# Kernel tuning notes

Measured on AMD Instinct MI355X. Metric: run time of the kernel, lower is better.

The kernel has to match this reference:

```python
import jax, jax.numpy as jnp
import numpy as np
import math

HEADS = 8
DIM_HEAD = 64


def setup_inputs() -> dict:
    key = jax.random.key(0)
    k1, k2, k3 = jax.random.split(key, 3)
    b, n, dim = 4, 2048, 512
    inner = HEADS * DIM_HEAD  # 512
    x = jax.random.normal(k1, (b, n, dim), dtype=jnp.float32)
    W_qkv = jax.random.normal(k2, (dim, 4 * inner), dtype=jnp.float32) * (dim ** -0.5)
    W_out = jax.random.normal(k3, (2 * inner, dim), dtype=jnp.float32) * ((2 * inner) ** -0.5)
    b_out = jnp.zeros((dim,), dtype=jnp.float32)
    return {"x": x, "W_qkv": W_qkv, "W_out": W_out, "b_out": b_out}


def reference(x, W_qkv, W_out, b_out):
    b, n, d = x.shape
    h, dh = HEADS, DIM_HEAD
    scale = dh ** -0.5
    qkvt = x @ W_qkv  # [b, n, 4*h*dh]
    q, k, v, t = jnp.split(qkvt, 4, axis=-1)
    # 'b n (h d) -> b h n d'
    def to_heads(z):
        return z.reshape(b, n, h, dh).transpose(0, 2, 1, 3)
    q, k, v, t = map(to_heads, (q, k, v, t))

    # Branch 1: standard softmax attention
    dots = jnp.einsum('bhid,bhjd->bhij', q, k) * scale
    attn1 = jax.nn.softmax(dots, axis=-1)
    out1 = jnp.einsum('bhij,bhjd->bhid', attn1, v)

    # Branch 2: fixed positional-decay attention (shared across b, h; no repeat needed)
    pos = jnp.arange(1, n + 1, dtype=x.dtype)  # linspace(1, n, n)
    tg = jnp.abs(pos[None, :] - pos[:, None])  # |j - i|, [n, n]
    attn2 = jnp.exp(-tg / jnp.asarray(math.e, dtype=x.dtype))
    # NOTE: original divides by sum(-1) WITHOUT keepdim -> broadcasts over columns:
    # attn2[i, j] / sum_k attn2[j, k]
    attn2 = attn2 / attn2.sum(-1)
    out2 = jnp.einsum('ij,bhjd->bhid', attn2, t)

    out = jnp.concatenate([out1, out2], axis=-1)  # [b, h, n, 2*dh]
    out = out.transpose(0, 2, 1, 3).reshape(b, n, 2 * h * dh)  # 'b h n d -> b n (h d)'
    return out @ W_out + b_out
```

## Files before the change

kernel.cpp:

```cpp
#include <hip/hip_runtime.h>
#include <hip/hip_bf16.h>

#define B_ 4
#define N_ 2048
#define D_ 512
#define H_ 8
#define DH_ 64

typedef float float4_ __attribute__((ext_vector_type(4)));
typedef int int2_ __attribute__((ext_vector_type(2)));
typedef int int4_ __attribute__((ext_vector_type(4)));
typedef unsigned short ushort4_ __attribute__((ext_vector_type(4)));
typedef unsigned short ushort8_ __attribute__((ext_vector_type(8)));
typedef __bf16 bf16x8 __attribute__((ext_vector_type(8)));
typedef _Float16 half2_ __attribute__((ext_vector_type(2)));
typedef _Float16 half4_ __attribute__((ext_vector_type(4)));
typedef _Float16 half8_ __attribute__((ext_vector_type(8)));

#if __has_builtin(__builtin_amdgcn_exp2f)
#define EXP2(x) __builtin_amdgcn_exp2f(x)
#else
#define EXP2(x) exp2f(x)
#endif

__device__ __forceinline__ float b2f(unsigned short u) {
  union { unsigned int u; float f; } v; v.u = ((unsigned int)u) << 16; return v.f;
}
__device__ __forceinline__ unsigned short f2b(float f) {
  union { float f; unsigned int u; } v; v.f = f;
  unsigned int r = v.u + 0x7fffu + ((v.u >> 16) & 1u);
  return (unsigned short)(r >> 16);
}
__device__ __forceinline__ half4_ pk4(float a, float b, float c, float d) {
  half2_ lo = __builtin_bit_cast(half2_, __builtin_amdgcn_cvt_pkrtz(a, b));
  half2_ hi = __builtin_bit_cast(half2_, __builtin_amdgcn_cvt_pkrtz(c, d));
  return __builtin_bit_cast(half4_,
      (int2_){__builtin_bit_cast(int, lo), __builtin_bit_cast(int, hi)});
}

#define GLD16(gp, lp)                                                        \
  __builtin_amdgcn_global_load_lds(                                          \
      (const __attribute__((address_space(1))) unsigned int*)(gp),           \
      (__attribute__((address_space(3))) unsigned int*)(lp), 16, 0, 0)

__device__ __forceinline__ bool detect_fp32_local(
    const unsigned short* __restrict__ xhdr, int* cnt_sh) {
  if (threadIdx.x == 0) *cnt_sh = 0;
  __syncthreads();
  unsigned int e = (xhdr[threadIdx.x] >> 7) & 0xFFu;
  if (e >= 134u) atomicAdd(cnt_sh, 1);
  __syncthreads();
  return *cnt_sh > 16;
}

__device__ __forceinline__ void transpose_conv(
    const void* __restrict__ src, unsigned short* __restrict__ dst,
    int R, int C, int bx, int by, bool ofp) {
  __shared__ unsigned short tile[32][33];
  const int c0 = bx * 32, r0 = by * 32;
  const int tx = threadIdx.x & 31, ty = threadIdx.x >> 5;
#pragma unroll
  for (int k = 0; k < 4; ++k) {
    int r = ty + k * 8;
    long idx = (long)(r0 + r) * C + c0 + tx;
    tile[r][tx] = ofp ? f2b(((const float*)src)[idx])
                      : ((const unsigned short*)src)[idx];
  }
  __syncthreads();
#pragma unroll
  for (int k = 0; k < 4; ++k) {
    int c = ty + k * 8;
    dst[(long)(c0 + c) * R + r0 + tx] = tile[tx][c];
  }
}

__global__ __launch_bounds__(256) void prep_all(
    const void* __restrict__ xraw, const void* __restrict__ Wqraw,
    const void* __restrict__ Woraw, unsigned short* __restrict__ xb,
    unsigned short* __restrict__ WqT, unsigned short* __restrict__ WoT,
    unsigned short* __restrict__ Wband) {
  __shared__ int cnt_sh;
  const bool ofp = detect_fp32_local((const unsigned short*)xraw, &cnt_sh);
  const int bid = blockIdx.x;
  if (bid < 4096) {
    int i4 = bid * 256 + threadIdx.x;
    ushort4_ o;
    if (ofp) {
      float4_ v = ((const float4_*)xraw)[i4];
      o[0] = f2b(v[0]); o[1] = f2b(v[1]); o[2] = f2b(v[2]); o[3] = f2b(v[3]);
    } else {
      o = ((const ushort4_*)xraw)[i4];
    }
    *(ushort4_*)(xb + (long)i4 * 4) = o;
  } else if (bid < 5120) {
    const int b2 = bid - 4096;
    transpose_conv(Wqraw, WqT, 512, 2048, b2 % 64, b2 / 64, ofp);
  } else if (bid < 5632) {
    const int b2 = bid - 5120;
    transpose_conv(Woraw, WoT, 1024, 512, b2 % 16, b2 / 16, ofp);
  } else {
    constexpr float INV_E = 0.36787944117144233f;
    constexpr float R1 = 0.69220062755534635f;
    constexpr float INV_1MR = 3.2488706f;
    const int i = bid - 5632;
    const int krel = threadIdx.x;
    const int j = (i >> 6) * 64 - 96 + krel;
    float c = 0.f;
    if (j >= 0 && j < N_) {
      float wgt = __expf(-fabsf((float)(i - j)) * INV_E);
      float rj = __expf(-(float)j * INV_E);
      float rnj = __expf(-(float)(N_ - 1 - j) * INV_E);
      float S = 1.f + R1 * (2.f - rj - rnj) * INV_1MR;
      c = wgt / S;
    }
    _Float16 hv = (_Float16)c;
    Wband[i * 256 + krel] = __builtin_bit_cast(unsigned short, hv);
  }
}

#define MFMA16x32(d, a, b) \
  d = __builtin_amdgcn_mfma_f32_16x16x32_bf16(a, b, d, 0, 0, 0)

__global__ __launch_bounds__(512, 2) void gemm256(
    const unsigned short* __restrict__ A, const unsigned short* __restrict__ Bt,
    unsigned short* __restrict__ C, int M, int N, int K) {
  __shared__ unsigned short As[2][16384];
  __shared__ unsigned short Bs[2][16384];
  const int tid = threadIdx.x;
  const int w = tid >> 6, lane = tid & 63, l16 = lane & 15, quad = lane >> 4;
  const int wm = w >> 2, wn = w & 3;
  const long tm = (long)blockIdx.x * 256, tn = (long)blockIdx.y * 256;

  const int srow = tid >> 3;
  const int sch = (tid & 7) ^ (srow & 7);
  const unsigned short* gA = A + (tm + srow) * (long)K + sch * 8;
  const unsigned short* gB = Bt + (tn + srow) * (long)K + sch * 8;

  const int xr8 = l16 & 7;
  const int ch0 = ((0 + quad) ^ xr8) * 8;
  const int ch1 = ((4 + quad) ^ xr8) * 8;
  const int rowA0 = (wm * 128 + l16) * 64;
  const int rowB0 = (wn * 64 + l16) * 64;

  float4_ acc[8][4] = {};

  auto stage = [&](int t, int bufn) __attribute__((always_inline)) {
#pragma unroll
    for (int r = 0; r < 4; ++r)
      GLD16(gA + (long)(r * 64) * K + t * 64, &As[bufn][r * 4096 + w * 512]);
#pragma unroll
    for (int r = 0; r < 4; ++r)
      GLD16(gB + (long)(r * 64) * K + t * 64, &Bs[bufn][r * 4096 + w * 512]);
  };

  stage(0, 0);
  asm volatile("s_waitcnt vmcnt(0)" ::: "memory");
  __builtin_amdgcn_s_barrier();

  const int NT = K >> 6;
  for (int t = 0; t < NT; ++t) {
    const int buf = t & 1;
    const unsigned short* as = As[buf];
    const unsigned short* bs = Bs[buf];
    bf16x8 af[8], bq[4], br[4];
#pragma unroll
    for (int mi = 0; mi < 4; ++mi) {
      af[mi * 2]     = __builtin_bit_cast(bf16x8, *(const int4_*)&as[rowA0 + mi * 1024 + ch0]);
      af[mi * 2 + 1] = __builtin_bit_cast(bf16x8, *(const int4_*)&as[rowA0 + mi * 1024 + ch1]);
    }
#pragma unroll
    for (int ni = 0; ni < 2; ++ni) {
      bq[ni * 2]     = __builtin_bit_cast(bf16x8, *(const int4_*)&bs[rowB0 + ni * 1024 + ch0]);
      bq[ni * 2 + 1] = __builtin_bit_cast(bf16x8, *(const int4_*)&bs[rowB0 + ni * 1024 + ch1]);
    }
    if (t + 1 < NT) stage(t + 1, buf ^ 1);
    __builtin_amdgcn_s_barrier();
    asm volatile("s_waitcnt lgkmcnt(0)" ::: "memory");
    __builtin_amdgcn_sched_barrier(0);
    __builtin_amdgcn_s_setprio(1);
#pragma unroll
    for (int mi = 0; mi < 4; ++mi)
#pragma unroll
      for (int ni = 0; ni < 2; ++ni) {
        MFMA16x32(acc[mi][ni], af[mi * 2], bq[ni * 2]);
        MFMA16x32(acc[mi][ni], af[mi * 2 + 1], bq[ni * 2 + 1]);
      }
    __builtin_amdgcn_s_setprio(0);
    __builtin_amdgcn_s_barrier();
#pragma unroll
    for (int ni = 0; ni < 2; ++ni) {
      br[ni * 2]     = __builtin_bit_cast(bf16x8, *(const int4_*)&bs[rowB0 + (2 + ni) * 1024 + ch0]);
      br[ni * 2 + 1] = __builtin_bit_cast(bf16x8, *(const int4_*)&bs[rowB0 + (2 + ni) * 1024 + ch1]);
    }
    __builtin_amdgcn_s_barrier();
    asm volatile("s_waitcnt lgkmcnt(0)" ::: "memory");
    __builtin_amdgcn_sched_barrier(0);
    __builtin_amdgcn_s_setprio(1);
#pragma unroll
    for (int mi = 0; mi < 4; ++mi)
#pragma unroll
      for (int ni = 0; ni < 2; ++ni) {
        MFMA16x32(acc[mi][2 + ni], af[mi * 2], br[ni * 2]);
        MFMA16x32(acc[mi][2 + ni], af[mi * 2 + 1], br[ni * 2 + 1]);
      }
    __builtin_amdgcn_s_setprio(0);
    __builtin_amdgcn_s_barrier();
#pragma unroll
    for (int mi = 0; mi < 4; ++mi) {
      af[mi * 2]     = __builtin_bit_cast(bf16x8, *(const int4_*)&as[rowA0 + (4 + mi) * 1024 + ch0]);
      af[mi * 2 + 1] = __builtin_bit_cast(bf16x8, *(const int4_*)&as[rowA0 + (4 + mi) * 1024 + ch1]);
    }
    __builtin_amdgcn_s_barrier();
    asm volatile("s_waitcnt lgkmcnt(0)" ::: "memory");
    __builtin_amdgcn_sched_barrier(0);
    __builtin_amdgcn_s_setprio(1);
#pragma unroll
    for (int mi = 0; mi < 4; ++mi)
#pragma unroll
      for (int ni = 0; ni < 2; ++ni) {
        MFMA16x32(acc[4 + mi][2 + ni], af[mi * 2], br[ni * 2]);
        MFMA16x32(acc[4 + mi][2 + ni], af[mi * 2 + 1], br[ni * 2 + 1]);
      }
    __builtin_amdgcn_s_setprio(0);
    __builtin_amdgcn_s_barrier();
#pragma unroll
    for (int ni = 0; ni < 2; ++ni) {
      bq[ni * 2]     = __builtin_bit_cast(bf16x8, *(const int4_*)&bs[rowB0 + ni * 1024 + ch0]);
      bq[ni * 2 + 1] = __builtin_bit_cast(bf16x8, *(const int4_*)&bs[rowB0 + ni * 1024 + ch1]);
    }
    __builtin_amdgcn_s_barrier();
    asm volatile("s_waitcnt lgkmcnt(0)" ::: "memory");
    __builtin_amdgcn_sched_barrier(0);
    __builtin_amdgcn_s_setprio(1);
#pragma unroll
    for (int mi = 0; mi < 4; ++mi)
#pragma unroll
      for (int ni = 0; ni < 2; ++ni) {
        MFMA16x32(acc[4 + mi][ni], af[mi * 2], bq[ni * 2]);
        MFMA16x32(acc[4 + mi][ni], af[mi * 2 + 1], bq[ni * 2 + 1]);
      }
    __builtin_amdgcn_s_setprio(0);
    asm volatile("s_waitcnt vmcnt(0)" ::: "memory");
    __builtin_amdgcn_sched_barrier(0);
    __builtin_amdgcn_s_barrier();
  }
#pragma unroll
  for (int ni = 0; ni < 4; ++ni) {
    long col = tn + wn * 64 + ni * 16 + l16;
#pragma unroll
    for (int mi = 0; mi < 8; ++mi)
#pragma unroll
      for (int r = 0; r < 4; ++r) {
        long row = tm + wm * 128 + mi * 16 + quad * 4 + r;
        C[row * N + col] = f2b(acc[mi][ni][r]);
      }
  }
}

__global__ __launch_bounds__(512, 2) void gemm_o(
    const unsigned short* __restrict__ A, const unsigned short* __restrict__ Bt,
    void* __restrict__ C, const void* __restrict__ bias_raw,
    const unsigned short* __restrict__ xhdr) {
  __shared__ int cnt_sh;
  const bool ofp = detect_fp32_local(xhdr, &cnt_sh);
  __shared__ unsigned short As[2][8192];
  __shared__ unsigned short Bs[2][8192];
  constexpr int K = 1024, N = 512;
  const int tid = threadIdx.x;
  const int w = tid >> 6, lane = tid & 63, l16 = lane & 15, quad = lane >> 4;
  const int wm = w >> 2, wn = w & 3;
  const long tm = (long)blockIdx.x * 128, tn = (long)blockIdx.y * 128;
  const int srow = tid >> 3;
  const int sch = (tid & 7) ^ (srow & 7);
  const unsigned short* gA = A + (tm + srow) * (long)K + sch * 8;
  const unsigned short* gB = Bt + (tn + srow) * (long)K + sch * 8;
  const int xr8 = l16 & 7;
  const int ch0 = ((0 + quad) ^ xr8) * 8;
  const int ch1 = ((4 + quad) ^ xr8) * 8;
  const int rowA0 = (wm * 64 + l16) * 64;
  const int rowB0 = (wn * 32 + l16) * 64;
  float4_ acc[4][2] = {};

  auto stage = [&](int t, int bufn) __attribute__((always_inline)) {
#pragma unroll
    for (int r = 0; r < 2; ++r)
      GLD16(gA + (long)(r * 64) * K + t * 64, &As[bufn][r * 4096 + w * 512]);
#pragma unroll
    for (int r = 0; r < 2; ++r)
      GLD16(gB + (long)(r * 64) * K + t * 64, &Bs[bufn][r * 4096 + w * 512]);
  };

  stage(0, 0);
  asm volatile("s_waitcnt vmcnt(0)" ::: "memory");
  __builtin_amdgcn_s_barrier();

  const int NT = K >> 6;
  for (int t = 0; t < NT; ++t) {
    const int buf = t & 1;
    const unsigned short* as = As[buf];
    const unsigned short* bs = Bs[buf];
    bf16x8 af[8], bf0[2], bf1[2];
#pragma unroll
    for (int mi = 0; mi < 4; ++mi) {
      af[mi * 2]     = __builtin_bit_cast(bf16x8, *(const int4_*)&as[rowA0 + mi * 1024 + ch0]);
      af[mi * 2 + 1] = __builtin_bit_cast(bf16x8, *(const int4_*)&as[rowA0 + mi * 1024 + ch1]);
    }
    bf0[0] = __builtin_bit_cast(bf16x8, *(const int4_*)&bs[rowB0 + ch0]);
    bf0[1] = __builtin_bit_cast(bf16x8, *(const int4_*)&bs[rowB0 + ch1]);
    if (t + 1 < NT) stage(t + 1, buf ^ 1);
    __builtin_amdgcn_s_barrier();
    asm volatile("s_waitcnt lgkmcnt(0)" ::: "memory");
    __builtin_amdgcn_sched_barrier(0);
    __builtin_amdgcn_s_setprio(1);
#pragma unroll
    for (int mi = 0; mi < 4; ++mi) {
      MFMA16x32(acc[mi][0], af[mi * 2], bf0[0]);
      MFMA16x32(acc[mi][0], af[mi * 2 + 1], bf0[1]);
    }
    __builtin_amdgcn_s_setprio(0);
    __builtin_amdgcn_s_barrier();
    bf1[0] = __builtin_bit_cast(bf16x8, *(const int4_*)&bs[rowB0 + 1024 + ch0]);
    bf1[1] = __builtin_bit_cast(bf16x8, *(const int4_*)&bs[rowB0 + 1024 + ch1]);
    __builtin_amdgcn_s_barrier();
    asm volatile("s_waitcnt lgkmcnt(0)" ::: "memory");
    __builtin_amdgcn_sched_barrier(0);
    __builtin_amdgcn_s_setprio(1);
#pragma unroll
    for (int mi = 0; mi < 4; ++mi) {
      MFMA16x32(acc[mi][1], af[mi * 2], bf1[0]);
      MFMA16x32(acc[mi][1], af[mi * 2 + 1], bf1[1]);
    }
    __builtin_amdgcn_s_setprio(0);
    asm volatile("s_waitcnt vmcnt(0)" ::: "memory");
    __builtin_amdgcn_sched_barrier(0);
    __builtin_amdgcn_s_barrier();
  }
#pragma unroll
  for (int nb = 0; nb < 2; ++nb) {
    long col = tn + wn * 32 + nb * 16 + l16;
    float bv = ofp ? ((const float*)bias_raw)[col]
                   : b2f(((const unsigned short*)bias_raw)[col]);
#pragma unroll
    for (int mb = 0; mb < 4; ++mb)
#pragma unroll
      for (int r = 0; r < 4; ++r) {
        long row = tm + wm * 64 + mb * 16 + quad * 4 + r;
        float val = acc[mb][nb][r] + bv;
        if (ofp) ((float*)C)[row * N + col] = val;
        else ((unsigned short*)C)[row * N + col] = f2b(val);
      }
  }
}

#define TSW 266
__global__ __launch_bounds__(256) void mid_all(
    const unsigned short* __restrict__ qkvt, unsigned short* __restrict__ Vt,
    const unsigned short* __restrict__ Wband, unsigned short* __restrict__ catb) {
  __shared__ __align__(16) unsigned short Ts[64 * TSW];
  const int bid = blockIdx.x;
  const int tid = threadIdx.x;
  if (bid < 512) {
    unsigned int* Td = (unsigned int*)Ts;
    const int bh = bid >> 4, b = bh >> 3, h = bh & 7;
    const int j0 = (bid & 15) * 128;
    const int dg = tid & 7;
#pragma unroll
    for (int it = 0; it < 2; ++it) {
      const int jp = (tid >> 3) + 32 * it;
      const long base =
          (long)(b * N_ + j0 + 2 * jp) * 2048 + 1024 + h * 64 + dg * 8;
      ushort8_ r0 = __builtin_bit_cast(ushort8_, *(const int4_*)&qkvt[base]);
      ushort8_ r1 = __builtin_bit_cast(ushort8_, *(const int4_*)&qkvt[base + 2048]);
#pragma unroll
      for (int e = 0; e < 8; ++e) {
        const int d = dg * 8 + e;
        const int S = (d >> 3) | ((d & 1) << 3);
        unsigned short h0 = __builtin_bit_cast(unsigned short, (_Float16)b2f(r0[e]));
        unsigned short h1 = __builtin_bit_cast(unsigned short, (_Float16)b2f(r1[e]));
        Td[d * 68 + (jp ^ (S << 2))] = (unsigned int)h0 | ((unsigned int)h1 << 16);
      }
    }
    __syncthreads();
#pragma unroll
    for (int it = 0; it < 4; ++it) {
      const int d = (tid >> 4) + 16 * it;
      const int ch = tid & 15;
      const int S = (d >> 3) | ((d & 1) << 3);
      int4_ v = *(const int4_*)&Td[d * 68 + ((ch ^ S) << 2)];
      *(int4_*)&Vt[((long)bh * 64 + d) * 2048 + j0 + ch * 8] = v;
    }
    return;
  }
  const int b2 = bid - 512;
  const int qtile = b2 & 31;
  const int bh = b2 >> 5, b = bh >> 3, h = bh & 7;
  const int jlo = qtile * 64 - 96;
  {
    unsigned int* Tsd = (unsigned int*)Ts;
    const int dg = tid & 7;
#pragma unroll
    for (int it = 0; it < 4; ++it) {
      const int kkp = (tid >> 3) + 32 * it;
      const int jA = jlo + 2 * kkp, jB = jA + 1;
      int4_ r0 = {}, r1 = {};
      if (jA >= 0 && jA < N_)
        r0 = *(const int4_*)&qkvt[(long)(b * N_ + jA) * 2048 + 1536 + h * 64 + dg * 8];
      if (jB >= 0 && jB < N_)
        r1 = *(const int4_*)&qkvt[(long)(b * N_ + jB) * 2048 + 1536 + h * 64 + dg * 8];
      ushort8_ u0 = __builtin_bit_cast(ushort8_, r0);
      ushort8_ u1 = __builtin_bit_cast(ushort8_, r1);
#pragma unroll
      for (int e = 0; e < 8; ++e) {
        const int d = dg * 8 + e;
        unsigned short h0 = __builtin_bit_cast(unsigned short, (_Float16)b2f(u0[e]));
        unsigned short h1 = __builtin_bit_cast(unsigned short, (_Float16)b2f(u1[e]));
        Tsd[d * 133 + kkp] = (unsigned int)h0 | ((unsigned int)h1 << 16);
      }
    }
  }
  __syncthreads();
  const int w = tid >> 6, lane = tid & 63, l16 = lane & 15, quad = lane >> 4;
  const int i_row = qtile * 64 + w * 16 + l16;
  const unsigned short* ap = Wband + i_row * 256;
  float4_ acc[4] = {};
#pragma unroll
  for (int kh = 0; kh < 8; ++kh) {
    half8_ af = __builtin_bit_cast(half8_, *(const int4_*)&ap[kh * 32 + quad * 8]);
#pragma unroll
    for (int nb = 0; nb < 4; ++nb) {
      half8_ bf = __builtin_bit_cast(half8_,
          *(const int4_*)&Ts[(nb * 16 + l16) * TSW + kh * 32 + quad * 8]);
      acc[nb] = __builtin_amdgcn_mfma_f32_16x16x32_f16(af, bf, acc[nb], 0, 0, 0);
    }
  }
#pragma unroll
  for (int nb = 0; nb < 4; ++nb)
#pragma unroll
    for (int r = 0; r < 4; ++r) {
      int row = qtile * 64 + w * 16 + quad * 4 + r;
      catb[(long)(b * N_ + row) * 1024 + h * 128 + 64 + nb * 16 + l16] =
          f2b(acc[nb][r]);
    }
}

__global__ __launch_bounds__(256) void flash_kernel(
    const unsigned short* __restrict__ qkvt, const unsigned short* __restrict__ Vt,
    unsigned short* __restrict__ catb) {
  __shared__ unsigned short Ks[2][64 * 64];
  __shared__ unsigned short Vs[2][64 * 64];
  const int flat = blockIdx.x + blockIdx.y * 16;
  const int slot = flat & 7, idx = flat >> 3;
  const int bh = slot * 4 + (idx >> 4);
  const int i0 = (idx & 15) * 128;
  const int b = bh >> 3, h = bh & 7;
  const int tid = threadIdx.x;
  const int w = tid >> 6, lane = tid & 63, l16 = lane & 15, quad = lane >> 4;
  const int srow8 = lane >> 3, sch = lane & 7;
  const int chK = sch ^ srow8;
  bf16x8 qf[2][2];
  {
    constexpr float SCL = 0.125f * 1.44269504088896f;
#pragma unroll
    for (int s2 = 0; s2 < 2; ++s2) {
      const long qrow =
          (long)(b * N_ + i0 + w * 32 + s2 * 16 + l16) * 2048 + h * 64;
#pragma unroll
      for (int kh = 0; kh < 2; ++kh) {
        ushort8_ raw = __builtin_bit_cast(ushort8_,
            *(const int4_*)&qkvt[qrow + kh * 32 + quad * 8]);
        ushort8_ sc;
#pragma unroll
        for (int e = 0; e < 8; ++e) sc[e] = f2b(b2f(raw[e]) * SCL);
        qf[s2][kh] = __builtin_bit_cast(bf16x8, sc);
      }
    }
  }
  const unsigned short* kp[2];
#pragma unroll
  for (int kh = 0; kh < 2; ++kh)
    kp[kh] = &Ks[0][l16 * 64 + (((kh * 4 + quad) ^ (l16 & 7)) * 8)];
  const unsigned short* vp[4];
#pragma unroll
  for (int c = 0; c < 4; ++c)
    vp[c] = &Vs[0][l16 * 64 + (((c * 2 + (quad >> 1)) ^ (l16 & 7)) * 8) +
                   (quad & 1) * 4];
  const unsigned short* kg[2];
  const unsigned short* vg[2];
#pragma unroll
  for (int g = 0; g < 2; ++g) {
    const int row = w * 16 + g * 8 + srow8;
    kg[g] = qkvt + (long)(b * N_ + row) * 2048 + 512 + h * 64 + chK * 8;
    vg[g] = Vt + ((long)bh * 64 + row) * 2048 + chK * 8;
  }
  float4_ O[2][4] = {};
  float4_ O5[2] = {};
  const half4_ ones = {(_Float16)1.f, (_Float16)1.f, (_Float16)1.f, (_Float16)1.f};

  auto stage = [&](int jt_, int buf_) __attribute__((always_inline)) {
    const int j0 = jt_ * 64;
#pragma unroll
    for (int g = 0; g < 2; ++g) {
      GLD16(kg[g] + (long)j0 * 2048,
            (char*)&Ks[0][0] + buf_ * 8192 + (w * 16 + g * 8) * 128);
      GLD16(vg[g] + j0,
            (char*)&Vs[0][0] + buf_ * 8192 + (w * 16 + g * 8) * 128);
    }
  };
  auto phase = [&](int jt_, int buf_) __attribute__((always_inline)) {
    if (jt_ + 1 < 32) stage(jt_ + 1, buf_ ^ 1);
    float4_ s[2][4] = {};
#pragma unroll
    for (int kh = 0; kh < 2; ++kh)
#pragma unroll
      for (int c = 0; c < 4; ++c) {
        bf16x8 kf = __builtin_bit_cast(bf16x8,
            *(const int4_*)(kp[kh] + buf_ * 4096 + c * 1024));
#pragma unroll
        for (int s2 = 0; s2 < 2; ++s2)
          s[s2][c] = __builtin_amdgcn_mfma_f32_16x16x32_bf16(
              kf, qf[s2][kh], s[s2][c], 0, 0, 0);
      }
    half4_ pf[2][4];
#pragma unroll
    for (int s2 = 0; s2 < 2; ++s2)
#pragma unroll
      for (int c = 0; c < 4; ++c)
        pf[s2][c] = pk4(EXP2(s[s2][c][0]), EXP2(s[s2][c][1]),
                        EXP2(s[s2][c][2]), EXP2(s[s2][c][3]));
#pragma unroll
    for (int c = 0; c < 4; ++c) {
#pragma unroll
      for (int dblk = 0; dblk < 4; ++dblk) {
        half4_ vfv = *(const half4_*)(vp[c] + buf_ * 4096 + dblk * 1024);
#pragma unroll
        for (int s2 = 0; s2 < 2; ++s2)
          O[s2][dblk] = __builtin_amdgcn_mfma_f32_16x16x16f16(
              pf[s2][c], vfv, O[s2][dblk], 0, 0, 0);
      }
#pragma unroll
      for (int s2 = 0; s2 < 2; ++s2)
        O5[s2] = __builtin_amdgcn_mfma_f32_16x16x16f16(
            pf[s2][c], ones, O5[s2], 0, 0, 0);
    }
    __syncthreads();
  };

  stage(0, 0);
  __syncthreads();
  for (int jt = 0; jt < 32; jt += 2) {
    phase(jt, 0);
    phase(jt + 1, 1);
  }
#pragma unroll
  for (int s2 = 0; s2 < 2; ++s2) {
    float linv[4];
#pragma unroll
    for (int r = 0; r < 4; ++r) linv[r] = 1.f / O5[s2][r];
#pragma unroll
    for (int dblk = 0; dblk < 4; ++dblk)
#pragma unroll
      for (int r = 0; r < 4; ++r) {
        int row = i0 + w * 32 + s2 * 16 + quad * 4 + r;
        catb[(long)(b * N_ + row) * 1024 + h * 128 + dblk * 16 + l16] =
            f2b(O[s2][dblk][r] * linv[r]);
      }
  }
}

extern "C" void kernel_launch(void* const* d_in, const int* in_sizes, int n_in,
                              void* d_out, int out_size, void* d_ws, size_t ws_size,
                              hipStream_t stream) {
  char* ws = (char*)d_ws;
  unsigned short* qkvt = (unsigned short*)(ws);
  unsigned short* WqT  = (unsigned short*)(ws + (size_t)32 * 1024 * 1024);
  unsigned short* WoT  = (unsigned short*)(ws + (size_t)34 * 1024 * 1024);
  unsigned short* Vt   = (unsigned short*)(ws + (size_t)35 * 1024 * 1024);
  unsigned short* catb = (unsigned short*)(ws + (size_t)43 * 1024 * 1024);
  unsigned short* xb   = (unsigned short*)(ws + (size_t)59 * 1024 * 1024);
  unsigned short* Wband= (unsigned short*)(ws + (size_t)68 * 1024 * 1024);

  prep_all<<<7680, 256, 0, stream>>>(d_in[0], d_in[1], d_in[2],
                                     xb, WqT, WoT, Wband);
  gemm256<<<dim3(8192 / 256, 2048 / 256), 512, 0, stream>>>(
      xb, WqT, qkvt, 8192, 2048, 512);
  mid_all<<<1536, 256, 0, stream>>>(qkvt, Vt, Wband, catb);
  flash_kernel<<<dim3(2048 / 128, 32), 256, 0, stream>>>(qkvt, Vt, catb);
  gemm_o<<<dim3(8192 / 128, 512 / 128), 512, 0, stream>>>(
      catb, WoT, d_out, d_in[3], (const unsigned short*)d_in[0]);
}
```

Baseline: 186.3 us.

## Software-pipeline attention loop: overlap QK^T of tile i with PV of tile i-1

Restructures the attention main loop so the QK^T MFMAs and exp for tile i are interleaved with the PV MFMAs of tile i-1, double-buffering the probability fragments in registers. K loads are staged one tile ahead, while V loads are issued one phase later, so V arrives just before use. The intent is to hide exp/VALU latency and the dependency between the score and PV MFMAs behind independent matrix work. It costs extra registers for the second pf buffer and makes the buffer indexing and barrier ordering more delicate.

After: 183.5 us. Within noise of the previous version (-1.5%).

```diff
diff --git a/kernel.cpp b/kernel.cpp
--- a/kernel.cpp
+++ b/kernel.cpp
@@ -496,61 +496,76 @@
   float4_ O5[2] = {};
   const half4_ ones = {(_Float16)1.f, (_Float16)1.f, (_Float16)1.f, (_Float16)1.f};
 
-  auto stage = [&](int jt_, int buf_) __attribute__((always_inline)) {
+  auto stage_k = [&](int jt_, int buf_) __attribute__((always_inline)) {
     const int j0 = jt_ * 64;
 #pragma unroll
-    for (int g = 0; g < 2; ++g) {
+    for (int g = 0; g < 2; ++g)
       GLD16(kg[g] + (long)j0 * 2048,
             (char*)&Ks[0][0] + buf_ * 8192 + (w * 16 + g * 8) * 128);
+  };
+  auto stage_v = [&](int jt_, int buf_) __attribute__((always_inline)) {
+    const int j0 = jt_ * 64;
+#pragma unroll
+    for (int g = 0; g < 2; ++g)
       GLD16(vg[g] + j0,
             (char*)&Vs[0][0] + buf_ * 8192 + (w * 16 + g * 8) * 128);
-    }
   };
-  auto phase = [&](int jt_, int buf_) __attribute__((always_inline)) {
-    if (jt_ + 1 < 32) stage(jt_ + 1, buf_ ^ 1);
+  auto pv_step = [&](half4_ (&pf)[2][4], int vb) __attribute__((always_inline)) {
+#pragma unroll
+    for (int c = 0; c < 4; ++c) {
+#pragma unroll
+      for (int dblk = 0; dblk < 4; ++dblk) {
+        half4_ vfv = *(const half4_*)(vp[c] + vb + dblk * 1024);
+#pragma unroll
+        for (int s2 = 0; s2 < 2; ++s2)
+          O[s2][dblk] = __builtin_amdgcn_mfma_f32_16x16x16f16(
+              pf[s2][c], vfv, O[s2][dblk], 0, 0, 0);
+      }
+#pragma unroll
+      for (int s2 = 0; s2 < 2; ++s2)
+        O5[s2] = __builtin_amdgcn_mfma_f32_16x16x16f16(
+            pf[s2][c], ones, O5[s2], 0, 0, 0);
+    }
+  };
+  auto phase = [&](int i, half4_ (&pfp)[2][4], half4_ (&pfc)[2][4],
+                   bool first, bool last) __attribute__((always_inline)) {
+    if (!last) stage_k(i + 1, (i + 1) & 1);
+    stage_v(i, i & 1);
+    const int kb = (i & 1) * 4096;
     float4_ s[2][4] = {};
 #pragma unroll
     for (int kh = 0; kh < 2; ++kh)
 #pragma unroll
       for (int c = 0; c < 4; ++c) {
         bf16x8 kf = __builtin_bit_cast(bf16x8,
-            *(const int4_*)(kp[kh] + buf_ * 4096 + c * 1024));
+            *(const int4_*)(kp[kh] + kb + c * 1024));
 #pragma unroll
         for (int s2 = 0; s2 < 2; ++s2)
           s[s2][c] = __builtin_amdgcn_mfma_f32_16x16x32_bf16(
               kf, qf[s2][kh], s[s2][c], 0, 0, 0);
       }
-    half4_ pf[2][4];
+    if (!first) pv_step(pfp, ((i - 1) & 1) * 4096);
 #pragma unroll
     for (int s2 = 0; s2 < 2; ++s2)
 #pragma unroll
       for (int c = 0; c < 4; ++c)
-        pf[s2][c] = pk4(EXP2(s[s2][c][0]), EXP2(s[s2][c][1]),
-                        EXP2(s[s2][c][2]), EXP2(s[s2][c][3]));
-#pragma unroll
-    for (int c = 0; c < 4; ++c) {
-#pragma unroll
-      for (int dblk = 0; dblk < 4; ++dblk) {
-        half4_ vfv = *(const half4_*)(vp[c] + buf_ * 4096 + dblk * 1024);
-#pragma unroll
-        for (int s2 = 0; s2 < 2; ++s2)
-          O[s2][dblk] = __builtin_amdgcn_mfma_f32_16x16x16f16(
-              pf[s2][c], vfv, O[s2][dblk], 0, 0, 0);
-      }
-#pragma unroll
-      for (int s2 = 0; s2 < 2; ++s2)
-        O5[s2] = __builtin_amdgcn_mfma_f32_16x16x16f16(
-            pf[s2][c], ones, O5[s2], 0, 0, 0);
-    }
+        pfc[s2][c] = pk4(EXP2(s[s2][c][0]), EXP2(s[s2][c][1]),
+                         EXP2(s[s2][c][2]), EXP2(s[s2][c][3]));
     __syncthreads();
   };
 
-  stage(0, 0);
-  __syncthreads();
-  for (int jt = 0; jt < 32; jt += 2) {
-    phase(jt, 0);
-    phase(jt + 1, 1);
-  }
+  half4_ pfA[2][4], pfB[2][4];
+  stage_k(0, 0);
+  asm volatile("s_waitcnt vmcnt(0)" ::: "memory");
+  __builtin_amdgcn_s_barrier();
+  phase(0, pfB, pfA, true, false);
+  for (int jt = 1; jt < 31; jt += 2) {
+    phase(jt, pfA, pfB, false, false);
+    phase(jt + 1, pfB, pfA, false, false);
+  }
+  phase(31, pfA, pfB, false, true);
+  pv_step(pfB, (31 & 1) * 4096);
+
 #pragma unroll
   for (int s2 = 0; s2 < 2; ++s2) {
     float linv[4];
```
